# Kernel optimization log

Hardware: AMD Instinct MI355X
Metric: run time of the kernel (lower is better)

The kernel has to match this reference:

```python
import jax, jax.numpy as jnp
import numpy as np

N, E, F_IN, DIM, HEADS = 16384, 262144, 128, 64, 4
HID = DIM * HEADS  # 256
NEG = 0.2


def _lin(k, fan_in, fan_out):
    kw, kb = jax.random.split(k)
    s = 1.0 / np.sqrt(fan_in)
    return (jax.random.uniform(kw, (fan_in, fan_out), jnp.float32, -s, s),
            jax.random.uniform(kb, (fan_out,), jnp.float32, -s, s))


def setup_inputs() -> dict:
    key = jax.random.key(0)
    ks = jax.random.split(key, 20)
    x = jax.random.normal(ks[0], (N, F_IN), jnp.float32)
    edge_index = jax.random.randint(ks[1], (2, E), 0, N, jnp.int32)
    Win, b_in = _lin(ks[2], F_IN, DIM)
    Wskip, bskip = _lin(ks[3], DIM, HID)
    # conv1: in=DIM, out per head=DIM, heads=HEADS, concat -> HID
    Wl1, _ = _lin(ks[4], DIM, HID)
    Wr1, _ = _lin(ks[5], DIM, HID)
    att1 = jax.random.normal(ks[6], (HEADS, DIM), jnp.float32) * 0.1
    b1 = jnp.zeros((HID,), jnp.float32)
    # conv2: in=HID, out=HID, heads=1, concat=False
    Wl2, _ = _lin(ks[7], HID, HID)
    Wr2, _ = _lin(ks[8], HID, HID)
    att2 = jax.random.normal(ks[9], (1, HID), jnp.float32) * 0.1
    b2 = jnp.zeros((HID,), jnp.float32)
    # conv3: in=HID, out=HID, heads=1, concat=False
    Wl3, _ = _lin(ks[10], HID, HID)
    Wr3, _ = _lin(ks[11], HID, HID)
    att3 = jax.random.normal(ks[12], (1, HID), jnp.float32) * 0.1
    b3 = jnp.zeros((HID,), jnp.float32)
    Wm1, bm1 = _lin(ks[13], HID, DIM)
    Wm2, bm2 = _lin(ks[14], DIM, DIM)
    Wm3, bm3 = _lin(ks[15], DIM, 1)
    return dict(x=x, edge_index=edge_index, Win=Win, b_in=b_in,
                Wskip=Wskip, bskip=bskip,
                Wl1=Wl1, Wr1=Wr1, att1=att1, b1=b1,
                Wl2=Wl2, Wr2=Wr2, att2=att2, b2=b2,
                Wl3=Wl3, Wr3=Wr3, att3=att3, b3=b3,
                Wm1=Wm1, bm1=bm1, Wm2=Wm2, bm2=bm2, Wm3=Wm3, bm3=bm3)


def gatv2(x, src, dst, Wl, Wr, att, b, concat):
    # PyG GATv2Conv: x_l = lin_l(x)[src], x_r = lin_r(x)[dst]
    n = x.shape[0]
    H, D = att.shape
    xl = (x @ Wl).reshape(n, H, D)
    xr = (x @ Wr).reshape(n, H, D)
    e = jax.nn.leaky_relu(xl[src] + xr[dst], NEG)          # [E, H, D]
    logits = jnp.einsum('ehd,hd->eh', e, att)              # [E, H]
    m = jax.ops.segment_max(logits, dst, num_segments=n)   # per-dst softmax
    alpha = jnp.exp(logits - m[dst])
    denom = jax.ops.segment_sum(alpha, dst, num_segments=n)
    alpha = alpha / denom[dst]
    out = jax.ops.segment_sum(alpha[:, :, None] * xl[src], dst, num_segments=n)
    out = out.reshape(n, H * D) if concat else out.mean(axis=1)
    return out + b


def reference(x, edge_index, Win, b_in, Wskip, bskip,
              Wl1, Wr1, att1, b1, Wl2, Wr2, att2, b2,
              Wl3, Wr3, att3, b3, Wm1, bm1, Wm2, bm2, Wm3, bm3):
    n = x.shape[0]
    # add self loops (GATv2Conv default add_self_loops=True)
    loop = jnp.arange(n, dtype=edge_index.dtype)
    src = jnp.concatenate([edge_index[0], loop])
    dst = jnp.concatenate([edge_index[1], loop])

    h = jax.nn.relu(x @ Win + b_in)                         # [N, DIM]
    out1 = jax.nn.relu(gatv2(h, src, dst, Wl1, Wr1, att1, b1, True))
    out1 = out1 + (h @ Wskip + bskip)                       # [N, HID]
    out2 = jax.nn.relu(gatv2(out1, src, dst, Wl2, Wr2, att2, b2, False))
    out2 = out2 + out1
    out3 = jax.nn.relu(gatv2(out2, src, dst, Wl3, Wr3, att3, b3, False))
    out3 = out3 + out2
    out = jax.nn.relu(out3 @ Wm1 + bm1)
    out = jax.nn.relu(out @ Wm2 + bm2)
    out = out @ Wm3 + bm3                                   # [N, 1]
    return out.reshape(-1)
```

## Files before the change

### kernel.cpp

```cpp
#include <hip/hip_runtime.h>
#include <cstdint>
#include <cstddef>

#define N_NODES 16384
#define E_EDGES 262144
#define FIN     128
#define DIM     64
#define HID     256
#define NEG     0.2f

typedef _Float16 h8 __attribute__((ext_vector_type(8)));
typedef _Float16 h4 __attribute__((ext_vector_type(4)));
typedef _Float16 h2 __attribute__((ext_vector_type(2)));
typedef float    f32x4 __attribute__((ext_vector_type(4)));

__global__ __launch_bounds__(256) void zero_cnt_kernel(int4* __restrict__ cnt) {
    cnt[blockIdx.x * 256 + threadIdx.x] = make_int4(0, 0, 0, 0);
}

__global__ __launch_bounds__(256) void hist_kernel(const int* __restrict__ dst,
                                                   int* __restrict__ cnt) {
    int i = blockIdx.x * 256 + threadIdx.x;
    if (i < E_EDGES) atomicAdd(&cnt[dst[i]], 1);
}

__global__ __launch_bounds__(256) void csr_scan_kernel(const int* __restrict__ cnt,
                                                       int* __restrict__ offs,
                                                       int* __restrict__ cursor) {
    __shared__ int bs[256];
    __shared__ int psum[257];
    int tid = threadIdx.x;
    int base = tid * 64;
    int s = 0;
    for (int i = 0; i < 64; ++i) s += cnt[base + i];
    bs[tid] = s;
    __syncthreads();
    if (tid == 0) {
        int r = 0;
        for (int i = 0; i < 256; ++i) { psum[i] = r; r += bs[i]; }
        psum[256] = r;
    }
    __syncthreads();
    int run = psum[tid];
    for (int i = 0; i < 64; ++i) {
        int c = cnt[base + i];
        offs[base + i] = run;
        cursor[base + i] = run;
        run += c;
    }
    if (tid == 255) offs[N_NODES] = run;
}

__global__ __launch_bounds__(256) void scatter_kernel(const int* __restrict__ src,
                                                      const int* __restrict__ dst,
                                                      int* __restrict__ cursor,
                                                      int* __restrict__ esrc) {
    int i = blockIdx.x * 256 + threadIdx.x;
    if (i < E_EDGES) {
        int p = atomicAdd(&cursor[dst[i]], 1);
        esrc[p] = src[i];
    }
}

struct PackJob { const float* W; _Float16* dst; int Ksrc, Nsrc, NT, colOff; };
struct PackJobs { PackJob j[10]; };

__global__ __launch_bounds__(256) void pack_all_kernel(PackJobs jobs) {
    PackJob jb = jobs.j[blockIdx.y];
    int i = blockIdx.x * 256 + threadIdx.x;
    if (i < jb.Ksrc * jb.Nsrc) {
        int k = i / jb.Nsrc, n = i % jb.Nsrc;
        jb.dst[((size_t)(k >> 3) * jb.NT + jb.colOff + n) * 8 + (k & 7)] = (_Float16)jb.W[i];
    }
}

template<int K, bool RELU, bool O16, bool IN32>
__global__ __launch_bounds__(64) void mfma_n64_kernel(const void* __restrict__ Av,
                                                      const _Float16* __restrict__ Wp,
                                                      const float* __restrict__ bias,
                                                      void* __restrict__ outv) {
    int lane = threadIdx.x;
    int rowBase = blockIdx.x * 64;
    int l15 = lane & 15, l4 = lane >> 4;

    f32x4 acc[4][4] = {};
#pragma unroll
    for (int ks = 0; ks < K / 32; ++ks) {
        h8 af[4], bf[4];
#pragma unroll
        for (int mi = 0; mi < 4; ++mi) {
            if constexpr (IN32) {
                const float* ap = (const float*)Av + (size_t)(rowBase + mi * 16 + l15) * K + ks * 32 + l4 * 8;
                float4 a0 = *(const float4*)ap;
                float4 a1 = *(const float4*)(ap + 4);
                h8 v;
                v[0] = (_Float16)a0.x; v[1] = (_Float16)a0.y;
                v[2] = (_Float16)a0.z; v[3] = (_Float16)a0.w;
                v[4] = (_Float16)a1.x; v[5] = (_Float16)a1.y;
                v[6] = (_Float16)a1.z; v[7] = (_Float16)a1.w;
                af[mi] = v;
            } else {
                af[mi] = *(const h8*)((const _Float16*)Av + (size_t)(rowBase + mi * 16 + l15) * K + ks * 32 + l4 * 8);
            }
        }
#pragma unroll
        for (int ni = 0; ni < 4; ++ni)
            bf[ni] = *(const h8*)(Wp + ((size_t)(ks * 4 + l4) * 64 + ni * 16 + l15) * 8);
#pragma unroll
        for (int mi = 0; mi < 4; ++mi)
#pragma unroll
            for (int ni = 0; ni < 4; ++ni)
                acc[mi][ni] = __builtin_amdgcn_mfma_f32_16x16x32_f16(af[mi], bf[ni], acc[mi][ni], 0, 0, 0);
    }
#pragma unroll
    for (int mi = 0; mi < 4; ++mi)
#pragma unroll
        for (int ni = 0; ni < 4; ++ni) {
            int c = ni * 16 + l15;
            float bv = bias[c];
#pragma unroll
            for (int q = 0; q < 4; ++q) {
                int r = rowBase + mi * 16 + l4 * 4 + q;
                float v = acc[mi][ni][q] + bv;
                if (RELU) v = fmaxf(v, 0.f);
                if constexpr (O16) ((_Float16*)outv)[(size_t)r * 64 + c] = (_Float16)v;
                else               ((float*)outv)[(size_t)r * 64 + c] = v;
            }
        }
}

template<int K>
__global__ __launch_bounds__(256) void mfma_gemm_kernel(const _Float16* __restrict__ A,
                                                        const _Float16* __restrict__ Wp,
                                                        int NT,
                                                        _Float16* __restrict__ o16a,
                                                        _Float16* __restrict__ o16b,
                                                        float* __restrict__ o32,
                                                        const float* __restrict__ bias) {
    int tid = threadIdx.x;
    int lane = tid & 63, wid = tid >> 6;
    int wm = wid >> 1, wn = wid & 1;
    int rowBase = blockIdx.x * 128 + wm * 64;
    int colBase = blockIdx.y * 128 + wn * 64;
    int l15 = lane & 15, l4 = lane >> 4;

    f32x4 acc[4][4] = {};
#pragma unroll
    for (int ks = 0; ks < K / 32; ++ks) {
        h8 af[4], bf[4];
#pragma unroll
        for (int mi = 0; mi < 4; ++mi)
            af[mi] = *(const h8*)(A + (size_t)(rowBase + mi * 16 + l15) * K + ks * 32 + l4 * 8);
#pragma unroll
        for (int ni = 0; ni < 4; ++ni)
            bf[ni] = *(const h8*)(Wp + ((size_t)(ks * 4 + l4) * NT + colBase + ni * 16 + l15) * 8);
#pragma unroll
        for (int mi = 0; mi < 4; ++mi)
#pragma unroll
            for (int ni = 0; ni < 4; ++ni)
                acc[mi][ni] = __builtin_amdgcn_mfma_f32_16x16x32_f16(af[mi], bf[ni], acc[mi][ni], 0, 0, 0);
    }

    int seg = colBase >> 8;
    int cbase = colBase & 255;
    if (o32 != nullptr && seg == 2) {
#pragma unroll
        for (int mi = 0; mi < 4; ++mi)
#pragma unroll
            for (int ni = 0; ni < 4; ++ni) {
                int c = cbase + ni * 16 + l15;
                float bv = bias[c];
#pragma unroll
                for (int q = 0; q < 4; ++q) {
                    int r = rowBase + mi * 16 + l4 * 4 + q;
                    o32[(size_t)r * 256 + c] = acc[mi][ni][q] + bv;
                }
            }
    } else {
        _Float16* o = (seg == 0) ? o16a : o16b;
#pragma unroll
        for (int mi = 0; mi < 4; ++mi)
#pragma unroll
            for (int ni = 0; ni < 4; ++ni) {
                int c = cbase + ni * 16 + l15;
#pragma unroll
                for (int q = 0; q < 4; ++q) {
                    int r = rowBase + mi * 16 + l4 * 4 + q;
                    o[(size_t)r * 256 + c] = (_Float16)acc[mi][ni][q];
                }
            }
    }
}

template<int H, int OMODE>
__global__ __launch_bounds__(256) void gat_agg_kernel(const _Float16* __restrict__ xl,
                                                      const _Float16* __restrict__ xr,
                                                      const float* __restrict__ att,
                                                      const float* __restrict__ bias,
                                                      const float* __restrict__ resid,
                                                      const int* __restrict__ offs,
                                                      const int* __restrict__ esrc,
                                                      float* __restrict__ out,
                                                      _Float16* __restrict__ out16) {
    int tid = threadIdx.x;
    int wid = tid >> 6;
    int lane = tid & 63;
    int node = blockIdx.x * 4 + wid;
    int g  = lane >> 4;
    int li = lane & 15;

    h2 xrv[8];
    {
        const h8* xp = (const h8*)(xr + ((size_t)node << 8) + (li << 4));
        h8 a0 = xp[0], a1 = xp[1];
#pragma unroll
        for (int i = 0; i < 4; ++i) { xrv[i][0] = a0[2 * i]; xrv[i][1] = a0[2 * i + 1]; }
#pragma unroll
        for (int i = 0; i < 4; ++i) { xrv[4 + i][0] = a1[2 * i]; xrv[4 + i][1] = a1[2 * i + 1]; }
    }
    h2 attv[8];
    {
        const float4* ap = (const float4*)(att + (li << 4));
#pragma unroll
        for (int i = 0; i < 4; ++i) {
            float4 a = ap[i];
            attv[2 * i][0] = (_Float16)a.x; attv[2 * i][1] = (_Float16)a.y;
            attv[2 * i + 1][0] = (_Float16)a.z; attv[2 * i + 1][1] = (_Float16)a.w;
        }
    }
    const h2 negc = { (_Float16)NEG, (_Float16)NEG };

    float m = -1e30f, s = 0.f;
    float acc[16];
#pragma unroll
    for (int i = 0; i < 16; ++i) acc[i] = 0.f;

    int e0 = offs[node];
    int total = offs[node + 1] - e0 + 1;

    for (int vi = g; vi < total; vi += 4) {
        int srcn = (vi == 0) ? node : esrc[e0 + vi - 1];
        const h8* xp = (const h8*)(xl + ((size_t)srcn << 8) + (li << 4));
        h8 a0 = xp[0], a1 = xp[1];

        float part = 0.f;
        float xf[16];
#pragma unroll
        for (int i = 0; i < 8; ++i) {
            h2 v;
            if (i < 4) { v[0] = a0[2 * i]; v[1] = a0[2 * i + 1]; }
            else       { v[0] = a1[2 * (i - 4)]; v[1] = a1[2 * (i - 4) + 1]; }
            xf[2 * i]     = (float)v[0];
            xf[2 * i + 1] = (float)v[1];
            h2 sum = v + xrv[i];
            h2 lr = __builtin_elementwise_max(sum, sum * negc);
            part = __builtin_amdgcn_fdot2(lr, attv[i], part, false);
        }
        part += __shfl_xor(part, 1);
        part += __shfl_xor(part, 2);
        if constexpr (H == 1) {
            part += __shfl_xor(part, 4);
            part += __shfl_xor(part, 8);
        }
        float lp = part;

        float mn = fmaxf(m, lp);
        float c = __expf(m - mn);
        float p = __expf(lp - mn);
        s = s * c + p;
#pragma unroll
        for (int i = 0; i < 16; ++i) acc[i] = acc[i] * c + p * xf[i];
        m = mn;
    }

#pragma unroll
    for (int mask = 16; mask <= 32; mask <<= 1) {
        float m2 = __shfl_xor(m, mask);
        float s2 = __shfl_xor(s, mask);
        float M = fmaxf(m, m2);
        float c1 = __expf(m - M);
        float c2 = __expf(m2 - M);
        s = s * c1 + s2 * c2;
#pragma unroll
        for (int i = 0; i < 16; ++i) {
            float a2 = __shfl_xor(acc[i], mask);
            acc[i] = acc[i] * c1 + a2 * c2;
        }
        m = M;
    }

    float inv = 1.f / s;
    int dbase = (li << 4) + (g << 2);
    float4 bv = *(const float4*)(bias + dbase);
    float4 rv = *(const float4*)(resid + ((size_t)node << 8) + dbase);
    float o0 = fmaxf(acc[(g << 2) + 0] * inv + bv.x, 0.f) + rv.x;
    float o1 = fmaxf(acc[(g << 2) + 1] * inv + bv.y, 0.f) + rv.y;
    float o2 = fmaxf(acc[(g << 2) + 2] * inv + bv.z, 0.f) + rv.z;
    float o3 = fmaxf(acc[(g << 2) + 3] * inv + bv.w, 0.f) + rv.w;
    if constexpr (OMODE != 2) {
        float4 ov = make_float4(o0, o1, o2, o3);
        *(float4*)(out + ((size_t)node << 8) + dbase) = ov;
    }
    if constexpr (OMODE != 0) {
        h4 hv;
        hv[0] = (_Float16)o0; hv[1] = (_Float16)o1;
        hv[2] = (_Float16)o2; hv[3] = (_Float16)o3;
        *(h4*)(out16 + ((size_t)node << 8) + dbase) = hv;
    }
}

__global__ __launch_bounds__(64) void mlp_head_kernel(const _Float16* __restrict__ A,
                                                      const _Float16* __restrict__ Wm1p,
                                                      const float* __restrict__ bm1,
                                                      const _Float16* __restrict__ Wm2p,
                                                      const float* __restrict__ bm2,
                                                      const float* __restrict__ Wm3,
                                                      const float* __restrict__ bm3,
                                                      float* __restrict__ out) {
    __shared__ _Float16 t1s[64][72];
    int lane = threadIdx.x;
    int rowBase = blockIdx.x * 64;
    int l15 = lane & 15, l4 = lane >> 4;

    f32x4 acc[4][4] = {};
#pragma unroll
    for (int ks = 0; ks < 8; ++ks) {
        h8 af[4], bf[4];
#pragma unroll
        for (int mi = 0; mi < 4; ++mi)
            af[mi] = *(const h8*)(A + (size_t)(rowBase + mi * 16 + l15) * 256 + ks * 32 + l4 * 8);
#pragma unroll
        for (int ni = 0; ni < 4; ++ni)
            bf[ni] = *(const h8*)(Wm1p + ((size_t)(ks * 4 + l4) * 64 + ni * 16 + l15) * 8);
#pragma unroll
        for (int mi = 0; mi < 4; ++mi)
#pragma unroll
            for (int ni = 0; ni < 4; ++ni)
                acc[mi][ni] = __builtin_amdgcn_mfma_f32_16x16x32_f16(af[mi], bf[ni], acc[mi][ni], 0, 0, 0);
    }
#pragma unroll
    for (int mi = 0; mi < 4; ++mi)
#pragma unroll
        for (int ni = 0; ni < 4; ++ni) {
            int c = ni * 16 + l15;
            float bv = bm1[c];
#pragma unroll
            for (int q = 0; q < 4; ++q)
                t1s[mi * 16 + l4 * 4 + q][c] = (_Float16)fmaxf(acc[mi][ni][q] + bv, 0.f);
        }

    f32x4 acc2[4][4] = {};
#pragma unroll
    for (int ks = 0; ks < 2; ++ks) {
        h8 af[4], bf[4];
#pragma unroll
        for (int mi = 0; mi < 4; ++mi)
            af[mi] = *(const h8*)&t1s[mi * 16 + l15][ks * 32 + l4 * 8];
#pragma unroll
        for (int ni = 0; ni < 4; ++ni)
            bf[ni] = *(const h8*)(Wm2p + ((size_t)(ks * 4 + l4) * 64 + ni * 16 + l15) * 8);
#pragma unroll
        for (int mi = 0; mi < 4; ++mi)
#pragma unroll
            for (int ni = 0; ni < 4; ++ni)
                acc2[mi][ni] = __builtin_amdgcn_mfma_f32_16x16x32_f16(af[mi], bf[ni], acc2[mi][ni], 0, 0, 0);
    }

    float b3 = bm3[0];
    float b2v[4], w3v[4];
#pragma unroll
    for (int ni = 0; ni < 4; ++ni) {
        b2v[ni] = bm2[ni * 16 + l15];
        w3v[ni] = Wm3[ni * 16 + l15];
    }
#pragma unroll
    for (int mi = 0; mi < 4; ++mi)
#pragma unroll
        for (int q = 0; q < 4; ++q) {
            float part = 0.f;
#pragma unroll
            for (int ni = 0; ni < 4; ++ni)
                part += fmaxf(acc2[mi][ni][q] + b2v[ni], 0.f) * w3v[ni];
            part += __shfl_xor(part, 1);
            part += __shfl_xor(part, 2);
            part += __shfl_xor(part, 4);
            part += __shfl_xor(part, 8);
            if (l15 == 0)
                out[rowBase + mi * 16 + l4 * 4 + q] = part + b3;
        }
}

extern "C" void kernel_launch(void* const* d_in, const int* in_sizes, int n_in,
                              void* d_out, int out_size, void* d_ws, size_t ws_size,
                              hipStream_t stream) {
    const float* x     = (const float*)d_in[0];
    const int*   ei    = (const int*)d_in[1];
    const float* Win   = (const float*)d_in[2];
    const float* b_in  = (const float*)d_in[3];
    const float* Wskip = (const float*)d_in[4];
    const float* bskip = (const float*)d_in[5];
    const float* Wl1   = (const float*)d_in[6];
    const float* Wr1   = (const float*)d_in[7];
    const float* att1  = (const float*)d_in[8];
    const float* b1    = (const float*)d_in[9];
    const float* Wl2   = (const float*)d_in[10];
    const float* Wr2   = (const float*)d_in[11];
    const float* att2  = (const float*)d_in[12];
    const float* b2    = (const float*)d_in[13];
    const float* Wl3   = (const float*)d_in[14];
    const float* Wr3   = (const float*)d_in[15];
    const float* att3  = (const float*)d_in[16];
    const float* b3    = (const float*)d_in[17];
    const float* Wm1   = (const float*)d_in[18];
    const float* bm1   = (const float*)d_in[19];
    const float* Wm2   = (const float*)d_in[20];
    const float* bm2   = (const float*)d_in[21];
    const float* Wm3   = (const float*)d_in[22];
    const float* bm3   = (const float*)d_in[23];

    char* p = (char*)d_ws;
    auto alloc = [&](size_t bytes) { char* r = p; p += (bytes + 255) & ~(size_t)255; return r; };
    const size_t NN = N_NODES;
    float*    skip = (float*)alloc(NN * 256 * 4);
    float*    out1 = (float*)alloc(NN * 256 * 4);
    _Float16* o116 = (_Float16*)alloc(NN * 256 * 2);
    _Float16* o216 = (_Float16*)alloc(NN * 256 * 2);
    _Float16* o316 = o116;
    _Float16* h16  = (_Float16*)alloc(NN * 64 * 2);
    _Float16* xl16 = (_Float16*)alloc(NN * 256 * 2);
    _Float16* xr16 = (_Float16*)alloc(NN * 256 * 2);
    _Float16* Wp1  = (_Float16*)alloc((size_t)64 * 768 * 2);
    _Float16* Wp2  = (_Float16*)alloc((size_t)256 * 512 * 2);
    _Float16* Wp3  = (_Float16*)alloc((size_t)256 * 512 * 2);
    _Float16* Winp = (_Float16*)alloc((size_t)128 * 64 * 2);
    _Float16* Wm1p = (_Float16*)alloc((size_t)256 * 64 * 2);
    _Float16* Wm2p = (_Float16*)alloc((size_t)64 * 64 * 2);
    int* cnt    = (int*)alloc(N_NODES * 4);
    int* offs   = (int*)alloc((N_NODES + 1) * 4);
    int* cursor = (int*)alloc(N_NODES * 4);
    int* esrc   = (int*)alloc(E_EDGES * 4);

    const int* src = ei;
    const int* dst = ei + E_EDGES;

    zero_cnt_kernel<<<N_NODES / 1024, 256, 0, stream>>>((int4*)cnt);
    hist_kernel<<<E_EDGES / 256, 256, 0, stream>>>(dst, cnt);
    csr_scan_kernel<<<1, 256, 0, stream>>>(cnt, offs, cursor);
    scatter_kernel<<<E_EDGES / 256, 256, 0, stream>>>(src, dst, cursor, esrc);

    PackJobs jobs = {{
        { Wl1,   Wp1,  64,  256, 768, 0   },
        { Wr1,   Wp1,  64,  256, 768, 256 },
        { Wskip, Wp1,  64,  256, 768, 512 },
        { Wl2,   Wp2,  256, 256, 512, 0   },
        { Wr2,   Wp2,  256, 256, 512, 256 },
        { Wl3,   Wp3,  256, 256, 512, 0   },
        { Wr3,   Wp3,  256, 256, 512, 256 },
        { Win,   Winp, 128, 64,  64,  0   },
        { Wm1,   Wm1p, 256, 64,  64,  0   },
        { Wm2,   Wm2p, 64,  64,  64,  0   },
    }};
    pack_all_kernel<<<dim3(256, 10), 256, 0, stream>>>(jobs);

    mfma_n64_kernel<128, true, true, true><<<N_NODES / 64, 64, 0, stream>>>(x, Winp, b_in, h16);

    mfma_gemm_kernel<64><<<dim3(128, 6), 256, 0, stream>>>(h16, Wp1, 768, xl16, xr16, skip, bskip);
    gat_agg_kernel<4, 1><<<N_NODES / 4, 256, 0, stream>>>(xl16, xr16, att1, b1, skip, offs, esrc, out1, o116);

    mfma_gemm_kernel<256><<<dim3(128, 4), 256, 0, stream>>>(o116, Wp2, 512, xl16, xr16, nullptr, nullptr);
    gat_agg_kernel<1, 1><<<N_NODES / 4, 256, 0, stream>>>(xl16, xr16, att2, b2, out1, offs, esrc, skip , o216);

    mfma_gemm_kernel<256><<<dim3(128, 4), 256, 0, stream>>>(o216, Wp3, 512, xl16, xr16, nullptr, nullptr);
    gat_agg_kernel<1, 2><<<N_NODES / 4, 256, 0, stream>>>(xl16, xr16, att3, b3, skip , offs, esrc, nullptr, o316);

    mlp_head_kernel<<<N_NODES / 64, 64, 0, stream>>>(o316, Wm1p, bm1, Wm2p, bm2, Wm3, bm3, (float*)d_out);
}
```

Before: 209.1 us.

## Unroll GAT edge loop two-wide and parallelize CSR scan with wave shuffles

The GATv2 aggregation loop now handles two edges per iteration. Both source rows are gathered before either logit is computed, and a single online-softmax rescale covers both, which raises memory-level parallelism and removes one exp per pair. Accumulators are stored as float2 vectors so the compiler can use packed FMA ops. Separately, the CSR scan kernel drops its serial single-thread prefix sum in favour of int4 loads, a wave shuffle scan and vectorized stores, at the cost of more registers per thread.

```diff
diff --git a/kernel.cpp b/kernel.cpp
--- a/kernel.cpp
+++ b/kernel.cpp
@@ -13,6 +13,7 @@
 typedef _Float16 h4 __attribute__((ext_vector_type(4)));
 typedef _Float16 h2 __attribute__((ext_vector_type(2)));
 typedef float    f32x4 __attribute__((ext_vector_type(4)));
+typedef float    f32x2 __attribute__((ext_vector_type(2)));
 
 __global__ __launch_bounds__(256) void zero_cnt_kernel(int4* __restrict__ cnt) {
     cnt[blockIdx.x * 256 + threadIdx.x] = make_int4(0, 0, 0, 0);
@@ -27,26 +28,39 @@
 __global__ __launch_bounds__(256) void csr_scan_kernel(const int* __restrict__ cnt,
                                                        int* __restrict__ offs,
                                                        int* __restrict__ cursor) {
-    __shared__ int bs[256];
-    __shared__ int psum[257];
-    int tid = threadIdx.x;
+    __shared__ int wsum[4];
+    int tid = threadIdx.x, lane = tid & 63, w = tid >> 6;
     int base = tid * 64;
+    const int4* c4 = (const int4*)(cnt + base);
+    int4 v[16];
     int s = 0;
-    for (int i = 0; i < 64; ++i) s += cnt[base + i];
-    bs[tid] = s;
+#pragma unroll
+    for (int i = 0; i < 16; ++i) {
+        v[i] = c4[i];
+        s += v[i].x + v[i].y + v[i].z + v[i].w;
+    }
+    int scan = s;
+#pragma unroll
+    for (int off = 1; off < 64; off <<= 1) {
+        int t = __shfl_up(scan, off);
+        if (lane >= off) scan += t;
+    }
+    if (lane == 63) wsum[w] = scan;
     __syncthreads();
-    if (tid == 0) {
-        int r = 0;
-        for (int i = 0; i < 256; ++i) { psum[i] = r; r += bs[i]; }
-        psum[256] = r;
-    }
-    __syncthreads();
-    int run = psum[tid];
-    for (int i = 0; i < 64; ++i) {
-        int c = cnt[base + i];
-        offs[base + i] = run;
-        cursor[base + i] = run;
-        run += c;
+    int wbase = 0;
+#pragma unroll
+    for (int i = 0; i < 4; ++i) if (i < w) wbase += wsum[i];
+    int run = wbase + (scan - s);
+#pragma unroll
+    for (int i = 0; i < 16; ++i) {
+        int4 o;
+        o.x = run;
+        o.y = o.x + v[i].x;
+        o.z = o.y + v[i].y;
+        o.w = o.z + v[i].z;
+        *(int4*)(offs + base + 4 * i) = o;
+        *(int4*)(cursor + base + 4 * i) = o;
+        run = o.w + v[i].w;
     }
     if (tid == 255) offs[N_NODES] = run;
 }
@@ -231,28 +245,26 @@
     const h2 negc = { (_Float16)NEG, (_Float16)NEG };
 
     float m = -1e30f, s = 0.f;
-    float acc[16];
-#pragma unroll
-    for (int i = 0; i < 16; ++i) acc[i] = 0.f;
+    f32x2 acc2[8];
+#pragma unroll
+    for (int i = 0; i < 8; ++i) acc2[i] = (f32x2){0.f, 0.f};
 
     int e0 = offs[node];
     int total = offs[node + 1] - e0 + 1;
 
-    for (int vi = g; vi < total; vi += 4) {
-        int srcn = (vi == 0) ? node : esrc[e0 + vi - 1];
+    auto gather = [&](int srcn, h2* hv) {
         const h8* xp = (const h8*)(xl + ((size_t)srcn << 8) + (li << 4));
         h8 a0 = xp[0], a1 = xp[1];
-
+#pragma unroll
+        for (int i = 0; i < 4; ++i) { hv[i][0] = a0[2 * i]; hv[i][1] = a0[2 * i + 1]; }
+#pragma unroll
+        for (int i = 0; i < 4; ++i) { hv[4 + i][0] = a1[2 * i]; hv[4 + i][1] = a1[2 * i + 1]; }
+    };
+    auto logit = [&](const h2* hv) -> float {
         float part = 0.f;
-        float xf[16];
 #pragma unroll
         for (int i = 0; i < 8; ++i) {
-            h2 v;
-            if (i < 4) { v[0] = a0[2 * i]; v[1] = a0[2 * i + 1]; }
-            else       { v[0] = a1[2 * (i - 4)]; v[1] = a1[2 * (i - 4) + 1]; }
-            xf[2 * i]     = (float)v[0];
-            xf[2 * i + 1] = (float)v[1];
-            h2 sum = v + xrv[i];
+            h2 sum = hv[i] + xrv[i];
             h2 lr = __builtin_elementwise_max(sum, sum * negc);
             part = __builtin_amdgcn_fdot2(lr, attv[i], part, false);
         }
@@ -262,14 +274,50 @@
             part += __shfl_xor(part, 4);
             part += __shfl_xor(part, 8);
         }
-        float lp = part;
-
+        return part;
+    };
+
+    int vi = g;
+    for (; vi + 4 < total; vi += 8) {
+        int sA = (vi == 0) ? node : esrc[e0 + vi - 1];
+        int sB = esrc[e0 + vi + 3];
+        h2 hA[8], hB[8];
+        gather(sA, hA);
+        gather(sB, hB);
+        float lpA = logit(hA);
+        float lpB = logit(hB);
+        float mn = fmaxf(m, fmaxf(lpA, lpB));
+        float c  = __expf(m - mn);
+        float pA = __expf(lpA - mn);
+        float pB = __expf(lpB - mn);
+        s = s * c + pA + pB;
+#pragma unroll
+        for (int i = 0; i < 8; ++i) {
+            f32x2 t = acc2[i] * c;
+            t[0] = fmaf(pA, (float)hA[i][0], t[0]);
+            t[1] = fmaf(pA, (float)hA[i][1], t[1]);
+            t[0] = fmaf(pB, (float)hB[i][0], t[0]);
+            t[1] = fmaf(pB, (float)hB[i][1], t[1]);
+            acc2[i] = t;
+        }
+        m = mn;
+    }
+    for (; vi < total; vi += 4) {
+        int srcn = (vi == 0) ? node : esrc[e0 + vi - 1];
+        h2 hA[8];
+        gather(srcn, hA);
+        float lp = logit(hA);
         float mn = fmaxf(m, lp);
         float c = __expf(m - mn);
         float p = __expf(lp - mn);
         s = s * c + p;
 #pragma unroll
-        for (int i = 0; i < 16; ++i) acc[i] = acc[i] * c + p * xf[i];
+        for (int i = 0; i < 8; ++i) {
+            f32x2 t = acc2[i] * c;
+            t[0] = fmaf(p, (float)hA[i][0], t[0]);
+            t[1] = fmaf(p, (float)hA[i][1], t[1]);
+            acc2[i] = t;
+        }
         m = mn;
     }
 
@@ -282,21 +330,28 @@
         float c2 = __expf(m2 - M);
         s = s * c1 + s2 * c2;
 #pragma unroll
-        for (int i = 0; i < 16; ++i) {
-            float a2 = __shfl_xor(acc[i], mask);
-            acc[i] = acc[i] * c1 + a2 * c2;
+        for (int i = 0; i < 8; ++i) {
+            float ax = __shfl_xor(acc2[i][0], mask);
+            float ay = __shfl_xor(acc2[i][1], mask);
+            acc2[i][0] = acc2[i][0] * c1 + ax * c2;
+            acc2[i][1] = acc2[i][1] * c1 + ay * c2;
         }
         m = M;
     }
 
     float inv = 1.f / s;
+    float a0, a1v, a2, a3;
+    if (g == 0)      { a0 = acc2[0][0]; a1v = acc2[0][1]; a2 = acc2[1][0]; a3 = acc2[1][1]; }
+    else if (g == 1) { a0 = acc2[2][0]; a1v = acc2[2][1]; a2 = acc2[3][0]; a3 = acc2[3][1]; }
+    else if (g == 2) { a0 = acc2[4][0]; a1v = acc2[4][1]; a2 = acc2[5][0]; a3 = acc2[5][1]; }
+    else             { a0 = acc2[6][0]; a1v = acc2[6][1]; a2 = acc2[7][0]; a3 = acc2[7][1]; }
     int dbase = (li << 4) + (g << 2);
     float4 bv = *(const float4*)(bias + dbase);
     float4 rv = *(const float4*)(resid + ((size_t)node << 8) + dbase);
-    float o0 = fmaxf(acc[(g << 2) + 0] * inv + bv.x, 0.f) + rv.x;
-    float o1 = fmaxf(acc[(g << 2) + 1] * inv + bv.y, 0.f) + rv.y;
-    float o2 = fmaxf(acc[(g << 2) + 2] * inv + bv.z, 0.f) + rv.z;
-    float o3 = fmaxf(acc[(g << 2) + 3] * inv + bv.w, 0.f) + rv.w;
+    float o0 = fmaxf(a0 * inv + bv.x, 0.f) + rv.x;
+    float o1 = fmaxf(a1v * inv + bv.y, 0.f) + rv.y;
+    float o2 = fmaxf(a2 * inv + bv.z, 0.f) + rv.z;
+    float o3 = fmaxf(a3 * inv + bv.w, 0.f) + rv.w;
     if constexpr (OMODE != 2) {
         float4 ov = make_float4(o0, o1, o2, o3);
         *(float4*)(out + ((size_t)node << 8) + dbase) = ov;
```

Result: faster. 198.7 us (-5.0%).
